# Optimization experiments

Hardware: AMD Instinct MI355X
Metric: run time of the kernel (lower is better)

The kernel has to match this reference:

```python
import jax, jax.numpy as jnp
import numpy as np

D = 1024
H = 16
HD = D // H
DFF = 4 * D
EPS = 1e-12


def setup_inputs() -> dict:
    key = jax.random.key(0)
    ks = jax.random.split(key, 16)
    s = lambda fan_in: 1.0 / np.sqrt(fan_in)
    inp = {
        "x": jax.random.normal(ks[0], (2, 2048, D), dtype=jnp.float32),
        "Wq": jax.random.normal(ks[1], (D, D), dtype=jnp.float32) * s(D),
        "bq": jax.random.normal(ks[2], (D,), dtype=jnp.float32) * 0.02,
        "Wk": jax.random.normal(ks[3], (D, D), dtype=jnp.float32) * s(D),
        "bk": jax.random.normal(ks[4], (D,), dtype=jnp.float32) * 0.02,
        "Wv": jax.random.normal(ks[5], (D, D), dtype=jnp.float32) * s(D),
        "bv": jax.random.normal(ks[6], (D,), dtype=jnp.float32) * 0.02,
        "Wo": jax.random.normal(ks[7], (D, D), dtype=jnp.float32) * s(D),
        "bo": jax.random.normal(ks[8], (D,), dtype=jnp.float32) * 0.02,
        "W1": jax.random.normal(ks[9], (D, DFF), dtype=jnp.float32) * s(D),
        "b1": jax.random.normal(ks[10], (DFF,), dtype=jnp.float32) * 0.02,
        "W2": jax.random.normal(ks[11], (DFF, D), dtype=jnp.float32) * s(DFF),
        "b2": jax.random.normal(ks[12], (D,), dtype=jnp.float32) * 0.02,
        "g1": jnp.ones((D,), dtype=jnp.float32),
        "s1": jnp.zeros((D,), dtype=jnp.float32),
        "g2": jnp.ones((D,), dtype=jnp.float32),
        "s2": jnp.zeros((D,), dtype=jnp.float32),
    }
    return inp


def _layer_norm(x, scale, shift):
    mean = jnp.mean(x, axis=-1, keepdims=True)
    # torch.var default is unbiased (ddof=1), matching the source module
    var = jnp.var(x, axis=-1, keepdims=True, ddof=1)
    return scale * (x - mean) / jnp.sqrt(var + EPS) + shift


def _gelu(x):
    c = jnp.sqrt(jnp.asarray(2.0 / np.pi, dtype=x.dtype))
    return 0.5 * x * (1.0 + jnp.tanh(c * (x + 0.044715 * x ** 3)))


def _block(x, Wq, bq, Wk, bk, Wv, bv, Wo, bo, W1, b1, W2, b2, g1, s1, g2, s2):
    B, S, _ = x.shape
    # pre-norm attention
    h = _layer_norm(x, g1, s1)
    q = (h @ Wq + bq).reshape(B, S, H, HD).transpose(0, 2, 1, 3)  # bhsd
    k = (h @ Wk + bk).reshape(B, S, H, HD).transpose(0, 2, 1, 3)
    v = (h @ Wv + bv).reshape(B, S, H, HD).transpose(0, 2, 1, 3)
    scores = jnp.einsum("bhqd,bhkd->bhqk", q, k)
    causal = jnp.tril(jnp.ones((S, S), dtype=bool))  # True = keep
    scores = jnp.where(causal, scores, -jnp.inf)
    attn = jax.nn.softmax(scores / np.sqrt(HD), axis=-1)
    ctx = jnp.einsum("bhqk,bhkd->bhqd", attn, v)
    ctx = ctx.transpose(0, 2, 1, 3).reshape(B, S, D)
    x = x + (ctx @ Wo + bo)
    # pre-norm MLP
    h = _layer_norm(x, g2, s2)
    h = _gelu(h @ W1 + b1) @ W2 + b2
    return x + h


def reference(x, Wq, bq, Wk, bk, Wv, bv, Wo, bo, W1, b1, W2, b2, g1, s1, g2, s2):
    return _block(x, Wq, bq, Wk, bk, Wv, bv, Wo, bo, W1, b1, W2, b2, g1, s1, g2, s2)
```

## Files before the change

kernel.cpp:

```cpp
#include <hip/hip_runtime.h>

#define D_ 1024
#define H_ 16
#define HD_ 64
#define DFF_ 4096
#define B_ 2
#define S_ 2048
#define MTOK 4096

typedef unsigned short u16;
typedef short bf16x8 __attribute__((ext_vector_type(8)));
typedef float f32x4 __attribute__((ext_vector_type(4)));

__device__ __forceinline__ u16 f2bf(float f) {
    union { float f; unsigned u; } v; v.f = f;
    return (u16)((v.u + 0x7fffu + ((v.u >> 16) & 1u)) >> 16);
}
__device__ __forceinline__ u16 f2bf_ru(float f) {
    union { float f; unsigned u; } v; v.f = f;
    return (u16)((v.u + 0x8000u) >> 16);
}

__device__ __forceinline__ void gload16(const void* g, void* l) {
    __builtin_amdgcn_global_load_lds(
        (const __attribute__((address_space(1))) unsigned int*)g,
        (__attribute__((address_space(3))) unsigned int*)l, 16, 0, 0);
}

__global__ __launch_bounds__(256) void transpose_cast_kernel(
    const float* __restrict__ W, u16* __restrict__ Wt, int K, int N) {
    __shared__ float t[32][33];
    int n0 = blockIdx.x * 32, k0 = blockIdx.y * 32;
    int tx = threadIdx.x, ty = threadIdx.y;
#pragma unroll
    for (int i = 0; i < 4; i++)
        t[ty + i * 8][tx] = W[(size_t)(k0 + ty + i * 8) * N + n0 + tx];
    __syncthreads();
#pragma unroll
    for (int i = 0; i < 4; i++)
        Wt[(size_t)(n0 + ty + i * 8) * K + k0 + tx] = f2bf(t[tx][ty + i * 8]);
}

__global__ __launch_bounds__(256) void ln_kernel(
    const float* __restrict__ x, const float* __restrict__ gamma,
    const float* __restrict__ beta, u16* __restrict__ out) {
    int row = blockIdx.x, tid = threadIdx.x;
    int wave = tid >> 6, lane = tid & 63;
    const float4* xr = (const float4*)(x + (size_t)row * D_);
    float4 v = xr[tid];
    float s = v.x + v.y + v.z + v.w;
#pragma unroll
    for (int off = 1; off < 64; off <<= 1) s += __shfl_xor(s, off, 64);
    __shared__ float p1[4], p2[4];
    if (lane == 0) p1[wave] = s;
    __syncthreads();
    float mean = (p1[0] + p1[1] + p1[2] + p1[3]) * (1.0f / D_);
    float4 d = {v.x - mean, v.y - mean, v.z - mean, v.w - mean};
    float sq = d.x * d.x + d.y * d.y + d.z * d.z + d.w * d.w;
#pragma unroll
    for (int off = 1; off < 64; off <<= 1) sq += __shfl_xor(sq, off, 64);
    if (lane == 0) p2[wave] = sq;
    __syncthreads();
    float var = (p2[0] + p2[1] + p2[2] + p2[3]) * (1.0f / (D_ - 1));
    float rstd = rsqrtf(var + 1e-12f);
    float4 gv = ((const float4*)gamma)[tid];
    float4 bv = ((const float4*)beta)[tid];
    u16* orow = out + (size_t)row * D_ + tid * 4;
    orow[0] = f2bf(gv.x * d.x * rstd + bv.x);
    orow[1] = f2bf(gv.y * d.y * rstd + bv.y);
    orow[2] = f2bf(gv.z * d.z * rstd + bv.z);
    orow[3] = f2bf(gv.w * d.w * rstd + bv.w);
}

constexpr int EPI_QKV = 0, EPI_O = 3, EPI_G = 4, EPI_R = 5;

template <int EPI, int KD, int TM>
__global__ __launch_bounds__(256) void gemm_kernel(
    const u16* __restrict__ A, const u16* __restrict__ Bt,
    const float* __restrict__ bias, const float* __restrict__ bias2,
    const float* __restrict__ bias3, const float* __restrict__ resid,
    void* __restrict__ Cout) {
    __shared__ alignas(16) u16 Alds[TM * 32];
    __shared__ alignas(16) u16 Blds[128 * 32];
    int tid = threadIdx.x;
    int tm = blockIdx.y * TM, tn = blockIdx.x * 128;
    int wave = tid >> 6, lane = tid & 63;
    int wrow = (wave >> 1) * (TM / 2), wcol = (wave & 1) * 64;
    int lrow = lane & 15, lk = (lane >> 4) * 8;
    constexpr int NI = TM / 32;
    f32x4 acc[NI][4] = {};
    const u16* ga = A + (size_t)(tm + (tid >> 2)) * KD + (tid & 3) * 8;
    const u16* gb = Bt + (size_t)(tn + (tid >> 2)) * KD + (tid & 3) * 8;
    char* lA = (char*)Alds + wave * 1024;
    char* lB = (char*)Blds + wave * 1024;
    for (int k0 = 0; k0 < KD; k0 += 32) {
        __syncthreads();
        gload16(ga + k0, lA);
        if constexpr (TM == 128) gload16(ga + (size_t)64 * KD + k0, lA + 4096);
        gload16(gb + k0, lB);
        gload16(gb + (size_t)64 * KD + k0, lB + 4096);
        __syncthreads();
        bf16x8 af[NI], bfr[4];
#pragma unroll
        for (int i = 0; i < NI; i++)
            af[i] = *(const bf16x8*)(Alds + (wrow + i * 16 + lrow) * 32 + lk);
#pragma unroll
        for (int j = 0; j < 4; j++)
            bfr[j] = *(const bf16x8*)(Blds + (wcol + j * 16 + lrow) * 32 + lk);
#pragma unroll
        for (int i = 0; i < NI; i++)
#pragma unroll
            for (int j = 0; j < 4; j++)
                acc[i][j] = __builtin_amdgcn_mfma_f32_16x16x32_bf16(
                    af[i], bfr[j], acc[i][j], 0, 0, 0);
    }
    int quad = lane >> 4, lcol = lane & 15;
#pragma unroll
    for (int i = 0; i < NI; i++)
#pragma unroll
        for (int j = 0; j < 4; j++)
#pragma unroll
            for (int r = 0; r < 4; r++) {
                int m = tm + wrow + i * 16 + quad * 4 + r;
                int n = tn + wcol + j * 16 + lcol;
                if constexpr (EPI == EPI_QKV) {
                    int which = n >> 10, d = n & 1023;
                    const float* bp = (which == 0) ? bias : (which == 1) ? bias2 : bias3;
                    float cval = acc[i][j][r] + bp[d];
                    int b = m >> 11, s = m & 2047, h = d >> 6, hd = d & 63;
                    u16* qkv = (u16*)Cout;
                    if (which == 0)
                        qkv[((size_t)(b * H_ + h) * S_ + s) * HD_ + hd] = f2bf(cval);
                    else if (which == 1)
                        qkv[4194304u + ((size_t)(b * H_ + h) * S_ + s) * HD_ + hd] = f2bf(cval);
                    else
                        qkv[8388608u + ((size_t)(b * H_ + h) * HD_ + hd) * S_ + s] = f2bf(cval);
                } else if constexpr (EPI == EPI_O) {
                    float cval = acc[i][j][r] + bias[n];
                    ((float*)Cout)[(size_t)m * D_ + n] = resid[(size_t)m * D_ + n] + cval;
                } else if constexpr (EPI == EPI_G) {
                    float cval = acc[i][j][r] + bias[n];
                    float u = 0.7978845608028654f * (cval + 0.044715f * cval * cval * cval);
                    float t = 1.0f - 2.0f / (__expf(2.0f * u) + 1.0f);
                    ((u16*)Cout)[(size_t)m * DFF_ + n] = f2bf(0.5f * cval * (1.0f + t));
                } else {
                    float cval = acc[i][j][r] + bias[n];
                    ((float*)Cout)[(size_t)m * D_ + n] = resid[(size_t)m * D_ + n] + cval;
                }
            }
}

__global__ __launch_bounds__(256) void attn_kernel(
    const u16* __restrict__ q, const u16* __restrict__ k,
    const u16* __restrict__ v, u16* __restrict__ ctx) {
    __shared__ alignas(16) u16 klds[2][64 * 64];
    __shared__ alignas(16) u16 vlds[2][64 * 64];
    __shared__ alignas(16) u16 plds[4][16 * 64];
    int tid = threadIdx.x, wave = tid >> 6, lane = tid & 63;
    int quad = lane >> 4, lcol = lane & 15;
    int bh = blockIdx.x & 31, pairi = blockIdx.x >> 5;
    const u16* qbase = q + (size_t)bh * S_ * HD_;
    const u16* kbase = k + (size_t)bh * S_ * HD_;
    const u16* vbase = v + (size_t)bh * HD_ * S_;
    int g = (lane & 7) ^ (lane >> 3);
    int srow = wave * 16 + (lane >> 3);
    const u16* kp = kbase + (size_t)srow * HD_ + g * 8;
    const u16* vp = vbase + (size_t)srow * S_ + g * 8;
    char* kd0 = (char*)klds[0] + wave * 2048;
    char* kd1 = (char*)klds[1] + wave * 2048;
    char* vd0 = (char*)vlds[0] + wave * 2048;
    char* vd1 = (char*)vlds[1] + wave * 2048;
    char* pbase = (char*)plds + wave * 2048;
    int koff0 = lcol * 128 + ((quad ^ (lcol & 7)) * 16);
    int koff1 = lcol * 128 + (((4 | quad) ^ (lcol & 7)) * 16);
    int b = bh >> 4, h = bh & 15;
#pragma unroll 1
    for (int half = 0; half < 2; half++) {
        int qt = half ? (31 - pairi) : pairi;
        int qr = qt * 64 + wave * 16;
        bf16x8 aq0 = *(const bf16x8*)(qbase + (size_t)(qr + lcol) * HD_ + quad * 8);
        bf16x8 aq1 = *(const bf16x8*)(qbase + (size_t)(qr + lcol) * HD_ + 32 + quad * 8);
        f32x4 co[4] = {};
        float li[4] = {0.0f, 0.0f, 0.0f, 0.0f};
        __syncthreads();
        gload16(kp, kd0);
        gload16(kp + (size_t)8 * HD_, kd0 + 1024);
        gload16(vp, vd0);
        gload16(vp + 8 * S_, vd0 + 1024);
        int cur = 0;
#pragma unroll 1
        for (int kt = 0; kt <= qt; kt++) {
            __syncthreads();
            if (kt < qt) {
                int k0 = (kt + 1) * 64;
                char* kd = cur ? kd0 : kd1;
                char* vd = cur ? vd0 : vd1;
                gload16(kp + (size_t)k0 * HD_, kd);
                gload16(kp + (size_t)(k0 + 8) * HD_, kd + 1024);
                gload16(vp + k0, vd);
                gload16(vp + 8 * S_ + k0, vd + 1024);
            }
            const u16* kl = klds[cur];
            const u16* vl = vlds[cur];
            f32x4 cs[4] = {};
#pragma unroll
            for (int j = 0; j < 4; j++) {
                bf16x8 bk = *(const bf16x8*)((char*)kl + j * 2048 + koff0);
                cs[j] = __builtin_amdgcn_mfma_f32_16x16x32_bf16(aq0, bk, cs[j], 0, 0, 0);
            }
#pragma unroll
            for (int j = 0; j < 4; j++) {
                bf16x8 bk = *(const bf16x8*)((char*)kl + j * 2048 + koff1);
                cs[j] = __builtin_amdgcn_mfma_f32_16x16x32_bf16(aq1, bk, cs[j], 0, 0, 0);
            }
            bool diag = (kt == qt);
#pragma unroll
            for (int r = 0; r < 4; r++) {
                int rr = quad * 4 + r;
                float p[4], ls = 0.0f;
#pragma unroll
                for (int j = 0; j < 4; j++) {
                    float sv = cs[j][r];
                    if (diag && (j * 16 + lcol > wave * 16 + rr)) sv = -1e38f;
                    p[j] = exp2f(sv * 0.18033688011112042f);
                    ls += p[j];
                }
                li[r] += ls;
                int pr = rr * 128 + (lcol & 7) * 2;
#pragma unroll
                for (int j = 0; j < 4; j++)
                    *(u16*)(pbase + pr + (((j * 2 + (lcol >> 3)) ^ (rr & 7)) * 16)) = f2bf_ru(p[j]);
            }
            {
                bf16x8 ap0 = *(const bf16x8*)(pbase + koff0);
                bf16x8 ap1 = *(const bf16x8*)(pbase + koff1);
#pragma unroll
                for (int j = 0; j < 4; j++) {
                    bf16x8 bv0 = *(const bf16x8*)((char*)vl + j * 2048 + koff0);
                    co[j] = __builtin_amdgcn_mfma_f32_16x16x32_bf16(ap0, bv0, co[j], 0, 0, 0);
                }
#pragma unroll
                for (int j = 0; j < 4; j++) {
                    bf16x8 bv1 = *(const bf16x8*)((char*)vl + j * 2048 + koff1);
                    co[j] = __builtin_amdgcn_mfma_f32_16x16x32_bf16(ap1, bv1, co[j], 0, 0, 0);
                }
            }
            cur ^= 1;
        }
#pragma unroll
        for (int r = 0; r < 4; r++) {
            float l = li[r];
            l += __shfl_xor(l, 1);
            l += __shfl_xor(l, 2);
            l += __shfl_xor(l, 4);
            l += __shfl_xor(l, 8);
            float inv = 1.0f / l;
            int row = qr + quad * 4 + r;
            size_t base = ((size_t)(b * S_ + row)) * D_ + h * HD_;
#pragma unroll
            for (int j = 0; j < 4; j++)
                ctx[base + j * 16 + lcol] = f2bf(co[j][r] * inv);
        }
    }
}

extern "C" void kernel_launch(void* const* d_in, const int* in_sizes, int n_in,
                              void* d_out, int out_size, void* d_ws, size_t ws_size,
                              hipStream_t stream) {
    const float* x  = (const float*)d_in[0];
    const float* Wq = (const float*)d_in[1];
    const float* bq = (const float*)d_in[2];
    const float* Wk = (const float*)d_in[3];
    const float* bk = (const float*)d_in[4];
    const float* Wv = (const float*)d_in[5];
    const float* bv = (const float*)d_in[6];
    const float* Wo = (const float*)d_in[7];
    const float* bo = (const float*)d_in[8];
    const float* W1 = (const float*)d_in[9];
    const float* b1 = (const float*)d_in[10];
    const float* W2 = (const float*)d_in[11];
    const float* b2 = (const float*)d_in[12];
    const float* g1 = (const float*)d_in[13];
    const float* s1 = (const float*)d_in[14];
    const float* g2 = (const float*)d_in[15];
    const float* s2 = (const float*)d_in[16];

    char* ws = (char*)d_ws;
    const size_t MB = 1024 * 1024;
    u16*   bWqkv = (u16*)(ws + 0 * MB);
    u16*   bWo   = (u16*)(ws + 6 * MB);
    u16*   bW1   = (u16*)(ws + 8 * MB);
    u16*   bW2   = (u16*)(ws + 16 * MB);
    u16*   hbuf  = (u16*)(ws + 24 * MB);
    u16*   qbuf  = (u16*)(ws + 32 * MB);
    u16*   ctxb  = (u16*)(ws + 56 * MB);
    float* x1    = (float*)(ws + 64 * MB);
    u16*   ffb   = (u16*)(ws + 80 * MB);

    dim3 tb(32, 8);
    transpose_cast_kernel<<<dim3(32, 32), tb, 0, stream>>>(Wq, bWqkv, D_, D_);
    transpose_cast_kernel<<<dim3(32, 32), tb, 0, stream>>>(Wk, bWqkv + 1024 * 1024, D_, D_);
    transpose_cast_kernel<<<dim3(32, 32), tb, 0, stream>>>(Wv, bWqkv + 2 * 1024 * 1024, D_, D_);
    transpose_cast_kernel<<<dim3(32, 32), tb, 0, stream>>>(Wo, bWo, D_, D_);
    transpose_cast_kernel<<<dim3(128, 32), tb, 0, stream>>>(W1, bW1, D_, DFF_);
    transpose_cast_kernel<<<dim3(32, 128), tb, 0, stream>>>(W2, bW2, DFF_, D_);

    ln_kernel<<<MTOK, 256, 0, stream>>>(x, g1, s1, hbuf);

    gemm_kernel<EPI_QKV, D_, 128><<<dim3(24, 32), 256, 0, stream>>>(
        hbuf, bWqkv, bq, bk, bv, nullptr, qbuf);

    attn_kernel<<<512, 256, 0, stream>>>(
        qbuf, qbuf + 4194304u, qbuf + 8388608u, ctxb);

    gemm_kernel<EPI_O, D_, 64><<<dim3(8, 64), 256, 0, stream>>>(
        ctxb, bWo, bo, nullptr, nullptr, x, x1);

    ln_kernel<<<MTOK, 256, 0, stream>>>(x1, g2, s2, hbuf);

    gemm_kernel<EPI_G, D_, 128><<<dim3(32, 32), 256, 0, stream>>>(
        hbuf, bW1, b1, nullptr, nullptr, nullptr, ffb);

    gemm_kernel<EPI_R, DFF_, 64><<<dim3(8, 64), 256, 0, stream>>>(
        ffb, bW2, b2, nullptr, nullptr, x1, (float*)d_out);
}
```

Before: 370.4 us.

## Swizzle GEMM LDS staging layout and remap block order for M-fastest rasterization

Adds an XOR swizzle to how global_load_lds stages A/B tiles into LDS, with a matching swizzled read address for the MFMA fragment loads, to avoid LDS bank conflicts on the bf16x8 reads. It also flattens the grid to 1D and decodes the M tile from the low bits of blockIdx.x, so consecutive blocks share the same weight column tile, which may improve L2 reuse of B. The swizzle has to match the per-wave direct-to-LDS write pattern exactly, or the results will be wrong.

New measurement: 368.0 us. About the same (-0.6%).

```diff
diff --git a/kernel.cpp b/kernel.cpp
--- a/kernel.cpp
+++ b/kernel.cpp
@@ -25,6 +25,13 @@
     __builtin_amdgcn_global_load_lds(
         (const __attribute__((address_space(1))) unsigned int*)g,
         (__attribute__((address_space(3))) unsigned int*)l, 16, 0, 0);
+}
+
+__device__ __forceinline__ void stage_src(int lane, int& rowoff, int& chunk) {
+    int l = lane >> 3, p = lane & 7;
+    int slog = p ^ l;
+    rowoff = l * 2 + (slog >> 2);
+    chunk = slog & 3;
 }
 
 __global__ __launch_bounds__(256) void transpose_cast_kernel(
@@ -74,7 +81,7 @@
 
 constexpr int EPI_QKV = 0, EPI_O = 3, EPI_G = 4, EPI_R = 5;
 
-template <int EPI, int KD, int TM>
+template <int EPI, int KD, int TM, int GYB>
 __global__ __launch_bounds__(256) void gemm_kernel(
     const u16* __restrict__ A, const u16* __restrict__ Bt,
     const float* __restrict__ bias, const float* __restrict__ bias2,
@@ -83,16 +90,20 @@
     __shared__ alignas(16) u16 Alds[TM * 32];
     __shared__ alignas(16) u16 Blds[128 * 32];
     int tid = threadIdx.x;
-    int tm = blockIdx.y * TM, tn = blockIdx.x * 128;
+    int tm = (blockIdx.x & ((1 << GYB) - 1)) * TM;
+    int tn = (blockIdx.x >> GYB) * 128;
     int wave = tid >> 6, lane = tid & 63;
     int wrow = (wave >> 1) * (TM / 2), wcol = (wave & 1) * 64;
-    int lrow = lane & 15, lk = (lane >> 4) * 8;
+    int lrow = lane & 15, quad = lane >> 4;
     constexpr int NI = TM / 32;
     f32x4 acc[NI][4] = {};
-    const u16* ga = A + (size_t)(tm + (tid >> 2)) * KD + (tid & 3) * 8;
-    const u16* gb = Bt + (size_t)(tn + (tid >> 2)) * KD + (tid & 3) * 8;
+    int sro, sch;
+    stage_src(lane, sro, sch);
+    const u16* ga = A + (size_t)(tm + wave * 16 + sro) * KD + sch * 8;
+    const u16* gb = Bt + (size_t)(tn + wave * 16 + sro) * KD + sch * 8;
     char* lA = (char*)Alds + wave * 1024;
     char* lB = (char*)Blds + wave * 1024;
+    int swz = (lrow >> 1) * 128 + (((((lrow & 1) << 2) | quad) ^ (lrow >> 1)) * 16);
     for (int k0 = 0; k0 < KD; k0 += 32) {
         __syncthreads();
         gload16(ga + k0, lA);
@@ -103,10 +114,10 @@
         bf16x8 af[NI], bfr[4];
 #pragma unroll
         for (int i = 0; i < NI; i++)
-            af[i] = *(const bf16x8*)(Alds + (wrow + i * 16 + lrow) * 32 + lk);
+            af[i] = *(const bf16x8*)((const char*)Alds + wrow * 64 + i * 1024 + swz);
 #pragma unroll
         for (int j = 0; j < 4; j++)
-            bfr[j] = *(const bf16x8*)(Blds + (wcol + j * 16 + lrow) * 32 + lk);
+            bfr[j] = *(const bf16x8*)((const char*)Blds + wcol * 64 + j * 1024 + swz);
 #pragma unroll
         for (int i = 0; i < NI; i++)
 #pragma unroll
@@ -114,7 +125,7 @@
                 acc[i][j] = __builtin_amdgcn_mfma_f32_16x16x32_bf16(
                     af[i], bfr[j], acc[i][j], 0, 0, 0);
     }
-    int quad = lane >> 4, lcol = lane & 15;
+    int lcol = lane & 15;
 #pragma unroll
     for (int i = 0; i < NI; i++)
 #pragma unroll
@@ -307,20 +318,20 @@
 
     ln_kernel<<<MTOK, 256, 0, stream>>>(x, g1, s1, hbuf);
 
-    gemm_kernel<EPI_QKV, D_, 128><<<dim3(24, 32), 256, 0, stream>>>(
+    gemm_kernel<EPI_QKV, D_, 128, 5><<<768, 256, 0, stream>>>(
         hbuf, bWqkv, bq, bk, bv, nullptr, qbuf);
 
     attn_kernel<<<512, 256, 0, stream>>>(
         qbuf, qbuf + 4194304u, qbuf + 8388608u, ctxb);
 
-    gemm_kernel<EPI_O, D_, 64><<<dim3(8, 64), 256, 0, stream>>>(
+    gemm_kernel<EPI_O, D_, 64, 6><<<512, 256, 0, stream>>>(
         ctxb, bWo, bo, nullptr, nullptr, x, x1);
 
     ln_kernel<<<MTOK, 256, 0, stream>>>(x1, g2, s2, hbuf);
 
-    gemm_kernel<EPI_G, D_, 128><<<dim3(32, 32), 256, 0, stream>>>(
+    gemm_kernel<EPI_G, D_, 128, 5><<<1024, 256, 0, stream>>>(
         hbuf, bW1, b1, nullptr, nullptr, nullptr, ffb);
 
-    gemm_kernel<EPI_R, DFF_, 64><<<dim3(8, 64), 256, 0, stream>>>(
+    gemm_kernel<EPI_R, DFF_, 64, 6><<<512, 256, 0, stream>>>(
         ffb, bW2, b2, nullptr, nullptr, x1, (float*)d_out);
 }
```

## Double-buffer GEMM LDS tiles with XOR swizzle, BK=64 option, and M-major block order

Applied to the files above, without the earlier changes.

Reworks the bf16 MFMA GEMM so the next K-tile is loaded asynchronously into a second LDS buffer while the current tile is consumed, which removes one barrier per iteration. It XOR-swizzles the LDS layout to cut bank conflicts on fragment reads and adds a BK=64 variant for the TM=64 GEMMs. It also flattens the grid so consecutive blocks walk M first and share the same B column tile. LDS use doubles, which may reduce occupancy, and the swizzle index math is easy to get wrong.

Measured after the change: 357.9 us. -3.4%, faster.

```diff
diff --git a/kernel.cpp b/kernel.cpp
--- a/kernel.cpp
+++ b/kernel.cpp
@@ -74,47 +74,106 @@
 
 constexpr int EPI_QKV = 0, EPI_O = 3, EPI_G = 4, EPI_R = 5;
 
-template <int EPI, int KD, int TM>
+template <int EPI, int KD, int TM, int BK, int GYB>
 __global__ __launch_bounds__(256) void gemm_kernel(
     const u16* __restrict__ A, const u16* __restrict__ Bt,
     const float* __restrict__ bias, const float* __restrict__ bias2,
     const float* __restrict__ bias3, const float* __restrict__ resid,
     void* __restrict__ Cout) {
-    __shared__ alignas(16) u16 Alds[TM * 32];
-    __shared__ alignas(16) u16 Blds[128 * 32];
+    __shared__ alignas(16) char Alds[2][TM * BK * 2];
+    __shared__ alignas(16) char Blds[2][128 * BK * 2];
     int tid = threadIdx.x;
-    int tm = blockIdx.y * TM, tn = blockIdx.x * 128;
+    int tm = (blockIdx.x & ((1 << GYB) - 1)) * TM;
+    int tn = (blockIdx.x >> GYB) * 128;
     int wave = tid >> 6, lane = tid & 63;
     int wrow = (wave >> 1) * (TM / 2), wcol = (wave & 1) * 64;
-    int lrow = lane & 15, lk = (lane >> 4) * 8;
+    int lcol = lane & 15, quad = lane >> 4;
     constexpr int NI = TM / 32;
     f32x4 acc[NI][4] = {};
-    const u16* ga = A + (size_t)(tm + (tid >> 2)) * KD + (tid & 3) * 8;
-    const u16* gb = Bt + (size_t)(tn + (tid >> 2)) * KD + (tid & 3) * 8;
-    char* lA = (char*)Alds + wave * 1024;
-    char* lB = (char*)Blds + wave * 1024;
-    for (int k0 = 0; k0 < KD; k0 += 32) {
+
+    const u16 *ga, *gb;
+    if constexpr (BK == 32) {
+        int l = lane >> 3, p = lane & 7, slog = p ^ l;
+        int sro = l * 2 + (slog >> 2), sch = slog & 3;
+        ga = A + (size_t)(tm + wave * 16 + sro) * KD + sch * 8;
+        gb = Bt + (size_t)(tn + wave * 16 + sro) * KD + sch * 8;
+    } else {
+        int g = (lane & 7) ^ (lane >> 3);
+        ga = A + (size_t)(tm + wave * 16 + (lane >> 3)) * KD + g * 8;
+        gb = Bt + (size_t)(tn + wave * 32 + (lane >> 3)) * KD + g * 8;
+    }
+
+    auto stage = [&](int k0, int buf) {
+        if constexpr (BK == 32) {
+            char* lA = Alds[buf] + wave * 1024;
+            char* lB = Blds[buf] + wave * 1024;
+            gload16(ga + k0, lA);
+            if constexpr (TM == 128) gload16(ga + (size_t)64 * KD + k0, lA + 4096);
+            gload16(gb + k0, lB);
+            gload16(gb + (size_t)64 * KD + k0, lB + 4096);
+        } else {
+            char* lA = Alds[buf] + wave * 2048;
+            gload16(ga + k0, lA);
+            gload16(ga + (size_t)8 * KD + k0, lA + 1024);
+            char* lB = Blds[buf] + wave * 4096;
+            gload16(gb + k0, lB);
+            gload16(gb + (size_t)8 * KD + k0, lB + 1024);
+            gload16(gb + (size_t)16 * KD + k0, lB + 2048);
+            gload16(gb + (size_t)24 * KD + k0, lB + 3072);
+        }
+    };
+
+    constexpr int NT = KD / BK;
+    stage(0, 0);
+    int cur = 0;
+#pragma unroll 1
+    for (int kt = 0; kt < NT; kt++) {
         __syncthreads();
-        gload16(ga + k0, lA);
-        if constexpr (TM == 128) gload16(ga + (size_t)64 * KD + k0, lA + 4096);
-        gload16(gb + k0, lB);
-        gload16(gb + (size_t)64 * KD + k0, lB + 4096);
-        __syncthreads();
-        bf16x8 af[NI], bfr[4];
-#pragma unroll
-        for (int i = 0; i < NI; i++)
-            af[i] = *(const bf16x8*)(Alds + (wrow + i * 16 + lrow) * 32 + lk);
-#pragma unroll
-        for (int j = 0; j < 4; j++)
-            bfr[j] = *(const bf16x8*)(Blds + (wcol + j * 16 + lrow) * 32 + lk);
-#pragma unroll
-        for (int i = 0; i < NI; i++)
+        if (kt + 1 < NT) stage((kt + 1) * BK, cur ^ 1);
+        if constexpr (BK == 32) {
+            int swz = (lcol >> 1) * 128 + (((((lcol & 1) << 2) | quad) ^ (lcol >> 1)) * 16);
+            bf16x8 af[NI], bfr[4];
+#pragma unroll
+            for (int i = 0; i < NI; i++)
+                af[i] = *(const bf16x8*)(Alds[cur] + wrow * 64 + i * 1024 + swz);
 #pragma unroll
             for (int j = 0; j < 4; j++)
-                acc[i][j] = __builtin_amdgcn_mfma_f32_16x16x32_bf16(
-                    af[i], bfr[j], acc[i][j], 0, 0, 0);
+                bfr[j] = *(const bf16x8*)(Blds[cur] + wcol * 64 + j * 1024 + swz);
+#pragma unroll
+            for (int i = 0; i < NI; i++)
+#pragma unroll
+                for (int j = 0; j < 4; j++)
+                    acc[i][j] = __builtin_amdgcn_mfma_f32_16x16x32_bf16(
+                        af[i], bfr[j], acc[i][j], 0, 0, 0);
+        } else {
+            int koff0 = lcol * 128 + ((quad ^ (lcol & 7)) * 16);
+            int koff1 = lcol * 128 + (((4 | quad) ^ (lcol & 7)) * 16);
+            bf16x8 af0[NI], af1[NI], bf0[4], bf1[4];
+#pragma unroll
+            for (int i = 0; i < NI; i++) {
+                af0[i] = *(const bf16x8*)(Alds[cur] + (wrow + i * 16) * 128 + koff0);
+                af1[i] = *(const bf16x8*)(Alds[cur] + (wrow + i * 16) * 128 + koff1);
+            }
+#pragma unroll
+            for (int j = 0; j < 4; j++) {
+                bf0[j] = *(const bf16x8*)(Blds[cur] + (wcol + j * 16) * 128 + koff0);
+                bf1[j] = *(const bf16x8*)(Blds[cur] + (wcol + j * 16) * 128 + koff1);
+            }
+#pragma unroll
+            for (int i = 0; i < NI; i++)
+#pragma unroll
+                for (int j = 0; j < 4; j++)
+                    acc[i][j] = __builtin_amdgcn_mfma_f32_16x16x32_bf16(
+                        af0[i], bf0[j], acc[i][j], 0, 0, 0);
+#pragma unroll
+            for (int i = 0; i < NI; i++)
+#pragma unroll
+                for (int j = 0; j < 4; j++)
+                    acc[i][j] = __builtin_amdgcn_mfma_f32_16x16x32_bf16(
+                        af1[i], bf1[j], acc[i][j], 0, 0, 0);
+        }
+        cur ^= 1;
     }
-    int quad = lane >> 4, lcol = lane & 15;
 #pragma unroll
     for (int i = 0; i < NI; i++)
 #pragma unroll
@@ -307,20 +366,20 @@
 
     ln_kernel<<<MTOK, 256, 0, stream>>>(x, g1, s1, hbuf);
 
-    gemm_kernel<EPI_QKV, D_, 128><<<dim3(24, 32), 256, 0, stream>>>(
+    gemm_kernel<EPI_QKV, D_, 128, 32, 5><<<768, 256, 0, stream>>>(
         hbuf, bWqkv, bq, bk, bv, nullptr, qbuf);
 
     attn_kernel<<<512, 256, 0, stream>>>(
         qbuf, qbuf + 4194304u, qbuf + 8388608u, ctxb);
 
-    gemm_kernel<EPI_O, D_, 64><<<dim3(8, 64), 256, 0, stream>>>(
+    gemm_kernel<EPI_O, D_, 64, 64, 6><<<512, 256, 0, stream>>>(
         ctxb, bWo, bo, nullptr, nullptr, x, x1);
 
     ln_kernel<<<MTOK, 256, 0, stream>>>(x1, g2, s2, hbuf);
 
-    gemm_kernel<EPI_G, D_, 128><<<dim3(32, 32), 256, 0, stream>>>(
+    gemm_kernel<EPI_G, D_, 128, 32, 5><<<1024, 256, 0, stream>>>(
         hbuf, bW1, b1, nullptr, nullptr, nullptr, ffb);
 
-    gemm_kernel<EPI_R, DFF_, 64><<<dim3(8, 64), 256, 0, stream>>>(
+    gemm_kernel<EPI_R, DFF_, 64, 64, 6><<<512, 256, 0, stream>>>(
         ffb, bW2, b2, nullptr, nullptr, x1, (float*)d_out);
 }
```
